# Optimization experiments

Measured on AMD Instinct MI355X. Metric: run time of the kernel, lower is better.

The kernel has to match this reference:

```python
import jax, jax.numpy as jnp
import numpy as np


def setup_inputs() -> dict:
    key = jax.random.key(0)
    kX, kA, kB, kC = jax.random.split(key, 4)
    Bsz, L, H, P, S = 2, 4096, 16, 64, 64
    X = jax.random.normal(kX, (Bsz, L, H, P), jnp.float32)
    # log-space negative decay per head (docstring: 'scalar decay per head (log space, negative)')
    A = -0.1 * jax.random.uniform(kA, (Bsz, L, H), jnp.float32)
    Bm = jax.random.normal(kB, (Bsz, L, H, S), jnp.float32) / np.sqrt(S).astype(np.float32)
    Cm = jax.random.normal(kC, (Bsz, L, H, S), jnp.float32) / np.sqrt(S).astype(np.float32)
    return {"X": X, "A": A, "B": Bm, "C": Cm, "chunk_size": 64}


def _ssd_forward(X, A, B, C, chunk_size):
    batch, seqlen, H, P = X.shape
    S = B.shape[-1]
    cs = chunk_size
    orig_seqlen = seqlen
    pad = (-seqlen) % cs
    if pad:
        X = jnp.pad(X, ((0, 0), (0, pad), (0, 0), (0, 0)))
        A = jnp.pad(A, ((0, 0), (0, pad), (0, 0)))
        B = jnp.pad(B, ((0, 0), (0, pad), (0, 0), (0, 0)))
        C = jnp.pad(C, ((0, 0), (0, pad), (0, 0), (0, 0)))
        seqlen = seqlen + pad
    n = seqlen // cs
    # reshape to chunks and move heads forward: [b, h, n, c, ...]
    Xc = X.reshape(batch, n, cs, H, P).transpose(0, 3, 1, 2, 4)
    Ac = A.reshape(batch, n, cs, H).transpose(0, 3, 1, 2)          # [b,h,n,c]
    Bc = B.reshape(batch, n, cs, H, S).transpose(0, 3, 1, 2, 4)
    Cc = C.reshape(batch, n, cs, H, S).transpose(0, 3, 1, 2, 4)
    Acs = jnp.cumsum(Ac, axis=-1)                                   # [b,h,n,c]
    # causal decay matrix L: exp(A_i - A_j) for i>=j; masked entries get -inf
    # then clamp(-inf, -100, 100) -> -100, exp(-100) ~ 3.7e-44 (faithful to torch order)
    diff = Acs[..., :, None] - Acs[..., None, :]                    # [b,h,n,c,c]
    causal = jnp.arange(cs)[:, None] >= jnp.arange(cs)[None, :]
    log_diff = jnp.clip(jnp.where(causal, diff, -jnp.inf), -100.0, 100.0)
    Lmat = jnp.nan_to_num(jnp.exp(log_diff), nan=0.0, posinf=1.0, neginf=0.0)
    # intra-chunk (attention-like) term
    CB = jnp.einsum('bhnis,bhnjs->bhnij', Cc, Bc)
    Y_intra = jnp.einsum('bhnij,bhnjp->bhnip', Lmat * CB, Xc)
    # inter-chunk state recurrence
    decay_chunk = jnp.exp(jnp.sum(Ac, axis=-1))                     # [b,h,n]
    decay_to_end = jnp.exp(Acs[..., -1:] - Acs)                     # [b,h,n,c]
    h_final = jnp.einsum('bhnc,bhncs,bhncp->bhnsp', decay_to_end, Bc, Xc)
    def step(carry, xs):
        d, hf = xs
        new_carry = d[..., None, None] * carry + hf
        return new_carry, carry  # h_inter[c] is state BEFORE chunk c
    d_scan = jnp.moveaxis(decay_chunk, 2, 0)                        # [n,b,h]
    h_scan = jnp.moveaxis(h_final, 2, 0)                            # [n,b,h,s,p]
    init = jnp.zeros((batch, H, S, P), X.dtype)
    _, h_inter = jax.lax.scan(step, init, (d_scan, h_scan))
    h_inter = jnp.moveaxis(h_inter, 0, 2)                           # [b,h,n,s,p]
    decay_from_start = jnp.exp(Acs)
    Y_inter = jnp.einsum('bhnis,bhnsp,bhni->bhnip', Cc, h_inter, decay_from_start)
    Y = (Y_intra + Y_inter).transpose(0, 2, 3, 1, 4).reshape(batch, seqlen, H, P)
    return Y[:, :orig_seqlen]


def reference(X, A, B, C, chunk_size):
    return _ssd_forward(X, A, B, C, chunk_size)
```

## Files before the change

### kernel.cpp

```cpp
#include <hip/hip_runtime.h>


#define BSZ 2
#define LSEQ 4096
#define NH 16
#define PP 64
#define SS 64
#define CS 64
#define NC (LSEQ / CS)
#define SCAN_G 8
#define HWS_ELEMS ((size_t)BSZ * NH * NC * SS * PP)

typedef float f32x4 __attribute__((ext_vector_type(4)));
typedef __bf16 bf16x8 __attribute__((ext_vector_type(8)));

union FragU { uint4 u; bf16x8 b; };

__device__ __forceinline__ unsigned short f2b(float x) {
    union { float f; unsigned u; } c; c.f = x;
    unsigned r = c.u + 0x7fffu + ((c.u >> 16) & 1u);
    return (unsigned short)(r >> 16);
}

__device__ __forceinline__ int rm_e(int row, int k) { return row * 64 + (k ^ ((row & 7) << 3)); }
__device__ __forceinline__ int tr_e(int row, int k) { return row * 64 + (k ^ (((row >> 1) & 7) << 3)); }

__device__ __forceinline__ bf16x8 frag_rm(const unsigned short* buf, int tile, int kk, int l) {
    const int row = tile * 16 + (l & 15);
    const int k = kk * 32 + ((l >> 4) << 3);
    FragU f; f.u = *(const uint4*)&buf[rm_e(row, k)];
    return f.b;
}
__device__ __forceinline__ bf16x8 frag_tr(const unsigned short* buf, int tile, int kk, int l) {
    const int row = tile * 16 + (l & 15);
    const int k = kk * 32 + ((l >> 4) << 3);
    FragU f; f.u = *(const uint4*)&buf[tr_e(row, k)];
    return f.b;
}

__global__ __launch_bounds__(256) void ssd_phase1(
    const float* __restrict__ Xg, const float* __restrict__ Ag,
    const float* __restrict__ Bg, const float* __restrict__ Cg,
    float* __restrict__ Yg, float* __restrict__ hws, float* __restrict__ dws)
{
    __shared__ __align__(16) unsigned short sB[64 * 64];
    __shared__ __align__(16) unsigned short sCM[64 * 64];
    __shared__ __align__(16) unsigned short sXt[64 * 64];
    __shared__ __align__(16) unsigned short sBt[64 * 64];
    __shared__ float sE[64], sR[64], sDte[64];

    const int tid = threadIdx.x;
    const int l = tid & 63;
    const int w = tid >> 6;
    const int n = blockIdx.x % NC;
    const int h = (blockIdx.x / NC) % NH;
    const int b = blockIdx.x / (NC * NH);
    const int row0 = b * LSEQ + n * CS;

    if (tid < 64) {
        float a = Ag[(size_t)(row0 + tid) * NH + h];
        #pragma unroll
        for (int off = 1; off < 64; off <<= 1) {
            float v = __shfl_up(a, off, 64);
            if (tid >= off) a += v;
        }
        sE[tid] = __expf(a);
        sR[tid] = __expf(-a);
        const float a63 = __shfl(a, 63, 64);
        sDte[tid] = __expf(a63 - a);
        if (tid == 63) dws[(b * NH + h) * NC + n] = __expf(a);
    }

    #pragma unroll
    for (int it = 0; it < 4; ++it) {
        const int c = (tid >> 4) + it * 16;
        const int p0 = (tid & 15) * 4;
        const size_t g = ((size_t)(row0 + c) * NH + h) * 64 + p0;
        const float4 xv = *(const float4*)&Xg[g];
        const float4 bv = *(const float4*)&Bg[g];
        const float4 cv = *(const float4*)&Cg[g];
        ushort4 bw; bw.x = f2b(bv.x); bw.y = f2b(bv.y); bw.z = f2b(bv.z); bw.w = f2b(bv.w);
        ushort4 cw; cw.x = f2b(cv.x); cw.y = f2b(cv.y); cw.z = f2b(cv.z); cw.w = f2b(cv.w);
        *(ushort4*)&sB[rm_e(c, p0)] = bw;
        *(ushort4*)&sCM[rm_e(c, p0)] = cw;
        sXt[tr_e(p0 + 0, c)] = f2b(xv.x);
        sXt[tr_e(p0 + 1, c)] = f2b(xv.y);
        sXt[tr_e(p0 + 2, c)] = f2b(xv.z);
        sXt[tr_e(p0 + 3, c)] = f2b(xv.w);
        sBt[tr_e(p0 + 0, c)] = bw.x;
        sBt[tr_e(p0 + 1, c)] = bw.y;
        sBt[tr_e(p0 + 2, c)] = bw.z;
        sBt[tr_e(p0 + 3, c)] = bw.w;
    }
    __syncthreads();

    const f32x4 zero = {0.f, 0.f, 0.f, 0.f};
    const int il = (l >> 4) << 2;

    f32x4 accCB[4] = {zero, zero, zero, zero};
    #pragma unroll
    for (int kk = 0; kk < 2; ++kk) {
        const bf16x8 aC = frag_rm(sCM, w, kk, l);
        #pragma unroll
        for (int tj = 0; tj < 4; ++tj) {
            const bf16x8 bB = frag_rm(sB, tj, kk, l);
            accCB[tj] = __builtin_amdgcn_mfma_f32_16x16x32_bf16(aC, bB, accCB[tj], 0, 0, 0);
        }
    }
    #pragma unroll
    for (int tj = 0; tj < 4; ++tj) {
        #pragma unroll
        for (int r = 0; r < 4; ++r) {
            const int i = w * 16 + il + r;
            const int j = tj * 16 + (l & 15);
            const float v = (i >= j) ? sE[i] * sR[j] * accCB[tj][r] : 0.f;
            sCM[i * 64 + (j ^ ((i & 7) << 3))] = f2b(v);
        }
    }

    f32x4 accY[4] = {zero, zero, zero, zero};
    f32x4 accH[4] = {zero, zero, zero, zero};
    #pragma unroll
    for (int kk = 0; kk < 2; ++kk) {
        const bf16x8 aM = frag_rm(sCM, w, kk, l);
        const bf16x8 aB = frag_tr(sBt, w, kk, l);
        const int c0 = kk * 32 + ((l >> 4) << 3);
        bf16x8 aBs;
        #pragma unroll
        for (int e = 0; e < 8; ++e) aBs[e] = (__bf16)((float)aB[e] * sDte[c0 + e]);
        #pragma unroll
        for (int tp = 0; tp < 4; ++tp) {
            const bf16x8 bX = frag_tr(sXt, tp, kk, l);
            accY[tp] = __builtin_amdgcn_mfma_f32_16x16x32_bf16(aM, bX, accY[tp], 0, 0, 0);
            accH[tp] = __builtin_amdgcn_mfma_f32_16x16x32_bf16(aBs, bX, accH[tp], 0, 0, 0);
        }
    }

    const size_t hb = ((size_t)(b * NH + h) * NC + n) * (size_t)(SS * PP);
    #pragma unroll
    for (int tp = 0; tp < 4; ++tp) {
        #pragma unroll
        for (int r = 0; r < 4; ++r) {
            const int i = w * 16 + il + r;
            const int p = tp * 16 + (l & 15);
            Yg[((size_t)(row0 + i) * NH + h) * 64 + p] = accY[tp][r];
            hws[hb + (size_t)i * 64 + p] = accH[tp][r];
        }
    }
}

__global__ __launch_bounds__(256) void ssd_scan(float* __restrict__ hws,
                                                const float* __restrict__ dws)
{
    __shared__ float sD[NC];
    const int tid = threadIdx.x;
    const int bh = blockIdx.x / SCAN_G;
    const int g = blockIdx.x % SCAN_G;
    if (tid < NC) sD[tid] = dws[bh * NC + tid];
    __syncthreads();

    float* base = hws + (size_t)bh * NC * (SS * PP) + g * (SS * PP / SCAN_G) + tid * 2;
    float cx = 0.f, cy = 0.f;
    for (int c = 0; c < NC; ++c) {
        const float d = sD[c];
        float2* p = (float2*)(base + (size_t)c * (SS * PP));
        const float2 hf = *p;
        float2 old; old.x = cx; old.y = cy;
        *p = old;
        cx = d * cx + hf.x;
        cy = d * cy + hf.y;
    }
}

__global__ __launch_bounds__(256) void ssd_phase3(
    const float* __restrict__ Ag, const float* __restrict__ Cg,
    const float* __restrict__ hws, float* __restrict__ Yg)
{
    __shared__ __align__(16) unsigned short sC[64 * 64];
    __shared__ __align__(16) unsigned short sHt[64 * 64];
    __shared__ float sE[64];

    const int tid = threadIdx.x;
    const int l = tid & 63;
    const int w = tid >> 6;
    const int n = blockIdx.x % NC;
    const int h = (blockIdx.x / NC) % NH;
    const int b = blockIdx.x / (NC * NH);
    const int row0 = b * LSEQ + n * CS;
    const size_t hb = ((size_t)(b * NH + h) * NC + n) * (size_t)(SS * PP);

    if (tid < 64) {
        float a = Ag[(size_t)(row0 + tid) * NH + h];
        #pragma unroll
        for (int off = 1; off < 64; off <<= 1) {
            float v = __shfl_up(a, off, 64);
            if (tid >= off) a += v;
        }
        sE[tid] = __expf(a);
    }

    #pragma unroll
    for (int it = 0; it < 4; ++it) {
        const int rr = (tid >> 4) + it * 16;
        const int p0 = (tid & 15) * 4;
        const float4 cv = *(const float4*)&Cg[((size_t)(row0 + rr) * NH + h) * 64 + p0];
        ushort4 cw; cw.x = f2b(cv.x); cw.y = f2b(cv.y); cw.z = f2b(cv.z); cw.w = f2b(cv.w);
        *(ushort4*)&sC[rm_e(rr, p0)] = cw;
        const float4 hv = *(const float4*)&hws[hb + (size_t)rr * 64 + p0];
        sHt[tr_e(p0 + 0, rr)] = f2b(hv.x);
        sHt[tr_e(p0 + 1, rr)] = f2b(hv.y);
        sHt[tr_e(p0 + 2, rr)] = f2b(hv.z);
        sHt[tr_e(p0 + 3, rr)] = f2b(hv.w);
    }
    __syncthreads();

    const f32x4 zero = {0.f, 0.f, 0.f, 0.f};
    f32x4 acc[4] = {zero, zero, zero, zero};
    #pragma unroll
    for (int kk = 0; kk < 2; ++kk) {
        const bf16x8 aC = frag_rm(sC, w, kk, l);
        #pragma unroll
        for (int tp = 0; tp < 4; ++tp) {
            const bf16x8 bH = frag_tr(sHt, tp, kk, l);
            acc[tp] = __builtin_amdgcn_mfma_f32_16x16x32_bf16(aC, bH, acc[tp], 0, 0, 0);
        }
    }

    const int il = (l >> 4) << 2;
    #pragma unroll
    for (int tp = 0; tp < 4; ++tp) {
        #pragma unroll
        for (int r = 0; r < 4; ++r) {
            const int i = w * 16 + il + r;
            const int p = tp * 16 + (l & 15);
            const size_t yo = ((size_t)(row0 + i) * NH + h) * 64 + p;
            Yg[yo] += sE[i] * acc[tp][r];
        }
    }
}

extern "C" void kernel_launch(void* const* d_in, const int* in_sizes, int n_in,
                              void* d_out, int out_size, void* d_ws, size_t ws_size,
                              hipStream_t stream) {
    const float* X = (const float*)d_in[0];
    const float* A = (const float*)d_in[1];
    const float* Bm = (const float*)d_in[2];
    const float* Cm = (const float*)d_in[3];
    float* Y = (float*)d_out;
    float* hws = (float*)d_ws;
    float* dws = hws + HWS_ELEMS;

    ssd_phase1<<<BSZ * NH * NC, 256, 0, stream>>>(X, A, Bm, Cm, Y, hws, dws);
    ssd_scan<<<BSZ * NH * SCAN_G, 256, 0, stream>>>(hws, dws);
    ssd_phase3<<<BSZ * NH * NC, 256, 0, stream>>>(A, Cm, hws, Y);
}
```

Before: 68.98 us.

## Store chunk states in bf16 and compute Y intra+inter in one final kernel

Restructures the three-kernel pipeline. The first kernel now computes only the per-chunk end states, writing them in bf16 and transposed. The scan works on packed bf16 pairs and prefetches the next chunk. The final kernel reloads X, B and C and computes the intra-chunk and inter-chunk terms together, writing Y once with float4 stores. This removes the Y write-then-read-modify-write and halves state-workspace traffic, at the cost of re-reading X and B in the last kernel and accumulating the scan recurrence from bf16-rounded values.

```diff
diff --git a/kernel.cpp b/kernel.cpp
--- a/kernel.cpp
+++ b/kernel.cpp
@@ -4,12 +4,9 @@
 #define BSZ 2
 #define LSEQ 4096
 #define NH 16
-#define PP 64
-#define SS 64
-#define CS 64
-#define NC (LSEQ / CS)
+#define NC 64
 #define SCAN_G 8
-#define HWS_ELEMS ((size_t)BSZ * NH * NC * SS * PP)
+#define HWS_ELEMS ((size_t)BSZ * NH * NC * 64 * 64)
 
 typedef float f32x4 __attribute__((ext_vector_type(4)));
 typedef __bf16 bf16x8 __attribute__((ext_vector_type(8)));
@@ -21,135 +18,100 @@
     unsigned r = c.u + 0x7fffu + ((c.u >> 16) & 1u);
     return (unsigned short)(r >> 16);
 }
+__device__ __forceinline__ float b2f(unsigned short v) {
+    union { unsigned u; float f; } c; c.u = ((unsigned)v) << 16;
+    return c.f;
+}
 
 __device__ __forceinline__ int rm_e(int row, int k) { return row * 64 + (k ^ ((row & 7) << 3)); }
 __device__ __forceinline__ int tr_e(int row, int k) { return row * 64 + (k ^ (((row >> 1) & 7) << 3)); }
 
 __device__ __forceinline__ bf16x8 frag_rm(const unsigned short* buf, int tile, int kk, int l) {
-    const int row = tile * 16 + (l & 15);
-    const int k = kk * 32 + ((l >> 4) << 3);
-    FragU f; f.u = *(const uint4*)&buf[rm_e(row, k)];
+    FragU f; f.u = *(const uint4*)&buf[rm_e(tile * 16 + (l & 15), kk * 32 + ((l >> 4) << 3))];
     return f.b;
 }
 __device__ __forceinline__ bf16x8 frag_tr(const unsigned short* buf, int tile, int kk, int l) {
-    const int row = tile * 16 + (l & 15);
-    const int k = kk * 32 + ((l >> 4) << 3);
-    FragU f; f.u = *(const uint4*)&buf[tr_e(row, k)];
+    FragU f; f.u = *(const uint4*)&buf[tr_e(tile * 16 + (l & 15), kk * 32 + ((l >> 4) << 3))];
     return f.b;
 }
 
-__global__ __launch_bounds__(256) void ssd_phase1(
+__global__ __launch_bounds__(256) void ssd_hfinal(
     const float* __restrict__ Xg, const float* __restrict__ Ag,
-    const float* __restrict__ Bg, const float* __restrict__ Cg,
-    float* __restrict__ Yg, float* __restrict__ hws, float* __restrict__ dws)
+    const float* __restrict__ Bg, unsigned short* __restrict__ hws,
+    float* __restrict__ dws)
 {
-    __shared__ __align__(16) unsigned short sB[64 * 64];
-    __shared__ __align__(16) unsigned short sCM[64 * 64];
+    __shared__ __align__(16) unsigned short sBt[64 * 64];
     __shared__ __align__(16) unsigned short sXt[64 * 64];
-    __shared__ __align__(16) unsigned short sBt[64 * 64];
-    __shared__ float sE[64], sR[64], sDte[64];
+    __shared__ float sDte[64];
 
     const int tid = threadIdx.x;
     const int l = tid & 63;
     const int w = tid >> 6;
-    const int n = blockIdx.x % NC;
-    const int h = (blockIdx.x / NC) % NH;
-    const int b = blockIdx.x / (NC * NH);
-    const int row0 = b * LSEQ + n * CS;
-
+    const int n = blockIdx.x & (NC - 1);
+    const int h = (blockIdx.x >> 6) & (NH - 1);
+    const int b = blockIdx.x >> 10;
+    const int row0 = b * LSEQ + n * 64;
+
+    float4 xv[4], bv[4];
+    const int p0 = (tid & 15) * 4;
+    #pragma unroll
+    for (int it = 0; it < 4; ++it) {
+        const int c = (tid >> 4) + it * 16;
+        const unsigned g = ((unsigned)(row0 + c) * NH + h) * 64 + p0;
+        xv[it] = *(const float4*)&Xg[g];
+        bv[it] = *(const float4*)&Bg[g];
+    }
     if (tid < 64) {
-        float a = Ag[(size_t)(row0 + tid) * NH + h];
+        float a = Ag[(unsigned)(row0 + tid) * NH + h];
         #pragma unroll
         for (int off = 1; off < 64; off <<= 1) {
             float v = __shfl_up(a, off, 64);
             if (tid >= off) a += v;
         }
-        sE[tid] = __expf(a);
-        sR[tid] = __expf(-a);
         const float a63 = __shfl(a, 63, 64);
         sDte[tid] = __expf(a63 - a);
-        if (tid == 63) dws[(b * NH + h) * NC + n] = __expf(a);
-    }
+        if (tid == 63) dws[(b * NH + h) * NC + n] = __expf(a63);
+    }
+    __syncthreads();
 
     #pragma unroll
     for (int it = 0; it < 4; ++it) {
         const int c = (tid >> 4) + it * 16;
-        const int p0 = (tid & 15) * 4;
-        const size_t g = ((size_t)(row0 + c) * NH + h) * 64 + p0;
-        const float4 xv = *(const float4*)&Xg[g];
-        const float4 bv = *(const float4*)&Bg[g];
-        const float4 cv = *(const float4*)&Cg[g];
-        ushort4 bw; bw.x = f2b(bv.x); bw.y = f2b(bv.y); bw.z = f2b(bv.z); bw.w = f2b(bv.w);
-        ushort4 cw; cw.x = f2b(cv.x); cw.y = f2b(cv.y); cw.z = f2b(cv.z); cw.w = f2b(cv.w);
-        *(ushort4*)&sB[rm_e(c, p0)] = bw;
-        *(ushort4*)&sCM[rm_e(c, p0)] = cw;
-        sXt[tr_e(p0 + 0, c)] = f2b(xv.x);
-        sXt[tr_e(p0 + 1, c)] = f2b(xv.y);
-        sXt[tr_e(p0 + 2, c)] = f2b(xv.z);
-        sXt[tr_e(p0 + 3, c)] = f2b(xv.w);
-        sBt[tr_e(p0 + 0, c)] = bw.x;
-        sBt[tr_e(p0 + 1, c)] = bw.y;
-        sBt[tr_e(p0 + 2, c)] = bw.z;
-        sBt[tr_e(p0 + 3, c)] = bw.w;
+        const float dte = sDte[c];
+        sBt[tr_e(p0 + 0, c)] = f2b(bv[it].x);
+        sBt[tr_e(p0 + 1, c)] = f2b(bv[it].y);
+        sBt[tr_e(p0 + 2, c)] = f2b(bv[it].z);
+        sBt[tr_e(p0 + 3, c)] = f2b(bv[it].w);
+        sXt[tr_e(p0 + 0, c)] = f2b(xv[it].x * dte);
+        sXt[tr_e(p0 + 1, c)] = f2b(xv[it].y * dte);
+        sXt[tr_e(p0 + 2, c)] = f2b(xv[it].z * dte);
+        sXt[tr_e(p0 + 3, c)] = f2b(xv[it].w * dte);
     }
     __syncthreads();
 
     const f32x4 zero = {0.f, 0.f, 0.f, 0.f};
-    const int il = (l >> 4) << 2;
-
-    f32x4 accCB[4] = {zero, zero, zero, zero};
+    f32x4 acc[4] = {zero, zero, zero, zero};
     #pragma unroll
     for (int kk = 0; kk < 2; ++kk) {
-        const bf16x8 aC = frag_rm(sCM, w, kk, l);
-        #pragma unroll
-        for (int tj = 0; tj < 4; ++tj) {
-            const bf16x8 bB = frag_rm(sB, tj, kk, l);
-            accCB[tj] = __builtin_amdgcn_mfma_f32_16x16x32_bf16(aC, bB, accCB[tj], 0, 0, 0);
-        }
-    }
-    #pragma unroll
-    for (int tj = 0; tj < 4; ++tj) {
-        #pragma unroll
-        for (int r = 0; r < 4; ++r) {
-            const int i = w * 16 + il + r;
-            const int j = tj * 16 + (l & 15);
-            const float v = (i >= j) ? sE[i] * sR[j] * accCB[tj][r] : 0.f;
-            sCM[i * 64 + (j ^ ((i & 7) << 3))] = f2b(v);
-        }
-    }
-
-    f32x4 accY[4] = {zero, zero, zero, zero};
-    f32x4 accH[4] = {zero, zero, zero, zero};
-    #pragma unroll
-    for (int kk = 0; kk < 2; ++kk) {
-        const bf16x8 aM = frag_rm(sCM, w, kk, l);
         const bf16x8 aB = frag_tr(sBt, w, kk, l);
-        const int c0 = kk * 32 + ((l >> 4) << 3);
-        bf16x8 aBs;
-        #pragma unroll
-        for (int e = 0; e < 8; ++e) aBs[e] = (__bf16)((float)aB[e] * sDte[c0 + e]);
-        #pragma unroll
-        for (int tp = 0; tp < 4; ++tp) {
-            const bf16x8 bX = frag_tr(sXt, tp, kk, l);
-            accY[tp] = __builtin_amdgcn_mfma_f32_16x16x32_bf16(aM, bX, accY[tp], 0, 0, 0);
-            accH[tp] = __builtin_amdgcn_mfma_f32_16x16x32_bf16(aBs, bX, accH[tp], 0, 0, 0);
-        }
-    }
-
-    const size_t hb = ((size_t)(b * NH + h) * NC + n) * (size_t)(SS * PP);
+        #pragma unroll
+        for (int tp = 0; tp < 4; ++tp)
+            acc[tp] = __builtin_amdgcn_mfma_f32_16x16x32_bf16(aB, frag_tr(sXt, tp, kk, l), acc[tp], 0, 0, 0);
+    }
+
+    const unsigned hb = ((unsigned)((b * NH + h) * NC + n)) * 4096u;
+    const int sbase = w * 16 + ((l >> 4) << 2);
     #pragma unroll
     for (int tp = 0; tp < 4; ++tp) {
-        #pragma unroll
-        for (int r = 0; r < 4; ++r) {
-            const int i = w * 16 + il + r;
-            const int p = tp * 16 + (l & 15);
-            Yg[((size_t)(row0 + i) * NH + h) * 64 + p] = accY[tp][r];
-            hws[hb + (size_t)i * 64 + p] = accH[tp][r];
-        }
-    }
-}
-
-__global__ __launch_bounds__(256) void ssd_scan(float* __restrict__ hws,
+        const int p = tp * 16 + (l & 15);
+        ushort4 o;
+        o.x = f2b(acc[tp][0]); o.y = f2b(acc[tp][1]);
+        o.z = f2b(acc[tp][2]); o.w = f2b(acc[tp][3]);
+        *(ushort4*)&hws[hb + (unsigned)p * 64 + sbase] = o;
+    }
+}
+
+__global__ __launch_bounds__(256) void ssd_scan(unsigned short* __restrict__ hws,
                                                 const float* __restrict__ dws)
 {
     __shared__ float sD[NC];
@@ -159,83 +121,132 @@
     if (tid < NC) sD[tid] = dws[bh * NC + tid];
     __syncthreads();
 
-    float* base = hws + (size_t)bh * NC * (SS * PP) + g * (SS * PP / SCAN_G) + tid * 2;
+    unsigned* hw32 = (unsigned*)hws;
+    const unsigned base = (unsigned)bh * NC * 2048u + g * 256u + tid;
     float cx = 0.f, cy = 0.f;
+    unsigned cur = hw32[base];
+    #pragma unroll 4
     for (int c = 0; c < NC; ++c) {
+        unsigned nxt = 0;
+        if (c < NC - 1) nxt = hw32[base + (c + 1) * 2048u];
+        const float hx = b2f((unsigned short)(cur & 0xffffu));
+        const float hy = b2f((unsigned short)(cur >> 16));
+        hw32[base + c * 2048u] = (unsigned)f2b(cx) | ((unsigned)f2b(cy) << 16);
         const float d = sD[c];
-        float2* p = (float2*)(base + (size_t)c * (SS * PP));
-        const float2 hf = *p;
-        float2 old; old.x = cx; old.y = cy;
-        *p = old;
-        cx = d * cx + hf.x;
-        cy = d * cy + hf.y;
-    }
-}
-
-__global__ __launch_bounds__(256) void ssd_phase3(
-    const float* __restrict__ Ag, const float* __restrict__ Cg,
-    const float* __restrict__ hws, float* __restrict__ Yg)
+        cx = d * cx + hx;
+        cy = d * cy + hy;
+        cur = nxt;
+    }
+}
+
+__global__ __launch_bounds__(256) void ssd_y(
+    const float* __restrict__ Xg, const float* __restrict__ Ag,
+    const float* __restrict__ Bg, const float* __restrict__ Cg,
+    const unsigned short* __restrict__ hws, float* __restrict__ Yg)
 {
+    __shared__ __align__(16) unsigned short sBM[64 * 64];
     __shared__ __align__(16) unsigned short sC[64 * 64];
-    __shared__ __align__(16) unsigned short sHt[64 * 64];
-    __shared__ float sE[64];
+    __shared__ __align__(16) unsigned short sXt[64 * 64];
+    __shared__ __align__(16) unsigned short sH[64 * 64];
+    __shared__ float sE[64], sR[64];
 
     const int tid = threadIdx.x;
     const int l = tid & 63;
     const int w = tid >> 6;
-    const int n = blockIdx.x % NC;
-    const int h = (blockIdx.x / NC) % NH;
-    const int b = blockIdx.x / (NC * NH);
-    const int row0 = b * LSEQ + n * CS;
-    const size_t hb = ((size_t)(b * NH + h) * NC + n) * (size_t)(SS * PP);
+    const int n = blockIdx.x & (NC - 1);
+    const int h = (blockIdx.x >> 6) & (NH - 1);
+    const int b = blockIdx.x >> 10;
+    const int row0 = b * LSEQ + n * 64;
+    const unsigned hb = ((unsigned)((b * NH + h) * NC + n)) * 4096u;
 
     if (tid < 64) {
-        float a = Ag[(size_t)(row0 + tid) * NH + h];
+        float a = Ag[(unsigned)(row0 + tid) * NH + h];
         #pragma unroll
         for (int off = 1; off < 64; off <<= 1) {
             float v = __shfl_up(a, off, 64);
             if (tid >= off) a += v;
         }
         sE[tid] = __expf(a);
-    }
-
-    #pragma unroll
-    for (int it = 0; it < 4; ++it) {
-        const int rr = (tid >> 4) + it * 16;
+        sR[tid] = __expf(-a);
+    }
+    {
         const int p0 = (tid & 15) * 4;
-        const float4 cv = *(const float4*)&Cg[((size_t)(row0 + rr) * NH + h) * 64 + p0];
-        ushort4 cw; cw.x = f2b(cv.x); cw.y = f2b(cv.y); cw.z = f2b(cv.z); cw.w = f2b(cv.w);
-        *(ushort4*)&sC[rm_e(rr, p0)] = cw;
-        const float4 hv = *(const float4*)&hws[hb + (size_t)rr * 64 + p0];
-        sHt[tr_e(p0 + 0, rr)] = f2b(hv.x);
-        sHt[tr_e(p0 + 1, rr)] = f2b(hv.y);
-        sHt[tr_e(p0 + 2, rr)] = f2b(hv.z);
-        sHt[tr_e(p0 + 3, rr)] = f2b(hv.w);
+        #pragma unroll
+        for (int it = 0; it < 4; ++it) {
+            const int c = (tid >> 4) + it * 16;
+            const unsigned g = ((unsigned)(row0 + c) * NH + h) * 64 + p0;
+            const float4 xv = *(const float4*)&Xg[g];
+            const float4 bv = *(const float4*)&Bg[g];
+            const float4 cv = *(const float4*)&Cg[g];
+            ushort4 bw; bw.x = f2b(bv.x); bw.y = f2b(bv.y); bw.z = f2b(bv.z); bw.w = f2b(bv.w);
+            ushort4 cw; cw.x = f2b(cv.x); cw.y = f2b(cv.y); cw.z = f2b(cv.z); cw.w = f2b(cv.w);
+            *(ushort4*)&sBM[rm_e(c, p0)] = bw;
+            *(ushort4*)&sC[rm_e(c, p0)] = cw;
+            sXt[tr_e(p0 + 0, c)] = f2b(xv.x);
+            sXt[tr_e(p0 + 1, c)] = f2b(xv.y);
+            sXt[tr_e(p0 + 2, c)] = f2b(xv.z);
+            sXt[tr_e(p0 + 3, c)] = f2b(xv.w);
+        }
+    }
+    {
+        const int pr = tid >> 2;
+        const int s0 = (tid & 3) * 16;
+        const uint4 h0 = *(const uint4*)&hws[hb + (unsigned)pr * 64 + s0];
+        const uint4 h1 = *(const uint4*)&hws[hb + (unsigned)pr * 64 + s0 + 8];
+        *(uint4*)&sH[rm_e(pr, s0)] = h0;
+        *(uint4*)&sH[rm_e(pr, s0 + 8)] = h1;
     }
     __syncthreads();
 
     const f32x4 zero = {0.f, 0.f, 0.f, 0.f};
-    f32x4 acc[4] = {zero, zero, zero, zero};
+    const int il = (l >> 4) << 2;
+
+    f32x4 accCB[4] = {zero, zero, zero, zero};
     #pragma unroll
     for (int kk = 0; kk < 2; ++kk) {
         const bf16x8 aC = frag_rm(sC, w, kk, l);
         #pragma unroll
-        for (int tp = 0; tp < 4; ++tp) {
-            const bf16x8 bH = frag_tr(sHt, tp, kk, l);
-            acc[tp] = __builtin_amdgcn_mfma_f32_16x16x32_bf16(aC, bH, acc[tp], 0, 0, 0);
-        }
-    }
-
-    const int il = (l >> 4) << 2;
-    #pragma unroll
-    for (int tp = 0; tp < 4; ++tp) {
+        for (int tj = 0; tj < 4; ++tj)
+            accCB[tj] = __builtin_amdgcn_mfma_f32_16x16x32_bf16(aC, frag_rm(sBM, tj, kk, l), accCB[tj], 0, 0, 0);
+    }
+    __syncthreads();
+
+    #pragma unroll
+    for (int tj = 0; tj < 4; ++tj) {
         #pragma unroll
         for (int r = 0; r < 4; ++r) {
             const int i = w * 16 + il + r;
-            const int p = tp * 16 + (l & 15);
-            const size_t yo = ((size_t)(row0 + i) * NH + h) * 64 + p;
-            Yg[yo] += sE[i] * acc[tp][r];
-        }
+            const int j = tj * 16 + (l & 15);
+            const float v = (i >= j) ? sE[i] * sR[j] * accCB[tj][r] : 0.f;
+            sBM[i * 64 + (j ^ ((i & 7) << 3))] = f2b(v);
+        }
+    }
+    __syncthreads();
+
+    f32x4 accY[4] = {zero, zero, zero, zero};
+    f32x4 accI[4] = {zero, zero, zero, zero};
+    #pragma unroll
+    for (int kk = 0; kk < 2; ++kk) {
+        const bf16x8 aX = frag_tr(sXt, w, kk, l);
+        const bf16x8 aH = frag_rm(sH, w, kk, l);
+        #pragma unroll
+        for (int ti = 0; ti < 4; ++ti) {
+            accY[ti] = __builtin_amdgcn_mfma_f32_16x16x32_bf16(aX, frag_rm(sBM, ti, kk, l), accY[ti], 0, 0, 0);
+            accI[ti] = __builtin_amdgcn_mfma_f32_16x16x32_bf16(aH, frag_rm(sC, ti, kk, l), accI[ti], 0, 0, 0);
+        }
+    }
+
+    const int pbase = w * 16 + il;
+    #pragma unroll
+    for (int ti = 0; ti < 4; ++ti) {
+        const int i = ti * 16 + (l & 15);
+        const float dfs = sE[i];
+        float4 o;
+        o.x = accY[ti][0] + dfs * accI[ti][0];
+        o.y = accY[ti][1] + dfs * accI[ti][1];
+        o.z = accY[ti][2] + dfs * accI[ti][2];
+        o.w = accY[ti][3] + dfs * accI[ti][3];
+        *(float4*)&Yg[((unsigned)(row0 + i) * NH + h) * 64 + pbase] = o;
     }
 }
 
@@ -247,10 +258,10 @@
     const float* Bm = (const float*)d_in[2];
     const float* Cm = (const float*)d_in[3];
     float* Y = (float*)d_out;
-    float* hws = (float*)d_ws;
-    float* dws = hws + HWS_ELEMS;
-
-    ssd_phase1<<<BSZ * NH * NC, 256, 0, stream>>>(X, A, Bm, Cm, Y, hws, dws);
+    unsigned short* hws = (unsigned short*)d_ws;
+    float* dws = (float*)(hws + HWS_ELEMS);
+
+    ssd_hfinal<<<BSZ * NH * NC, 256, 0, stream>>>(X, A, Bm, hws, dws);
     ssd_scan<<<BSZ * NH * SCAN_G, 256, 0, stream>>>(hws, dws);
-    ssd_phase3<<<BSZ * NH * NC, 256, 0, stream>>>(A, Cm, hws, Y);
-}
+    ssd_y<<<BSZ * NH * NC, 256, 0, stream>>>(X, A, Bm, Cm, hws, Y);
+}
```

After: 57.33 us. -16.9%, faster.
